# Kernel tuning notes

Measured on AMD Instinct MI355X. Metric: run time of the kernel, lower is better.

Reference implementation:

```python
import jax, jax.numpy as jnp
import numpy as np
from jax import lax

B_, H_, W_, C_ = 32, 56, 56, 256
RED = 16          # channel-attention reduction ratio
STATE = 16        # S6 state size
EPS = 1e-5        # BatchNorm eps


def setup_inputs() -> dict:
    key = jax.random.key(0)
    ks = jax.random.split(key, 10)
    x = jax.random.normal(ks[0], (B_, H_, W_, C_), jnp.float32)
    # ChannelAttention 1x1 convs (bias=False): C -> C/RED -> C
    ca_w1 = jax.random.normal(ks[1], (C_ // RED, C_), jnp.float32) * 0.05
    ca_w2 = jax.random.normal(ks[2], (C_, C_ // RED), jnp.float32) * 0.05
    # LSA 7x7 conv, 2 in-channels -> 1 out, HWIO layout
    lsa_w = jax.random.normal(ks[3], (7, 7, 2, 1), jnp.float32) * 0.05
    # S6 (d_model=1, state=STATE) parameters
    A = -jnp.exp(jax.random.normal(ks[4], (1, STATE), jnp.float32) * 0.5)  # negative for stable scan
    d_w = jax.random.normal(ks[5], (1, 1), jnp.float32) * 0.5
    d_b = jnp.zeros((1,), jnp.float32)
    B_w = jax.random.normal(ks[6], (STATE, 1), jnp.float32) * 0.5
    B_b = jnp.zeros((STATE,), jnp.float32)
    C_w = jax.random.normal(ks[7], (STATE, 1), jnp.float32) * 0.5
    C_b = jnp.zeros((STATE,), jnp.float32)
    bn_gamma = jnp.ones((C_,), jnp.float32)
    bn_beta = jnp.zeros((C_,), jnp.float32)
    return dict(x=x, ca_w1=ca_w1, ca_w2=ca_w2, lsa_w=lsa_w, A=A, d_w=d_w, d_b=d_b,
                B_w=B_w, B_b=B_b, C_w=C_w, C_b=C_b, bn_gamma=bn_gamma, bn_beta=bn_beta)


def _s6(m, A, d_w, d_b, B_w, B_b, C_w, C_b):
    # m: (B, L, 1) -- selective scan with d_model=1, state STATE
    delta = jax.nn.softplus(m @ d_w.T + d_b)          # (B,L,1)
    Bm = m @ B_w.T + B_b                              # (B,L,S)
    Cm = m @ C_w.T + C_b                              # (B,L,S)
    dA = jnp.exp(delta[..., None] * A)                # (B,L,1,S)
    dBx = (delta * m)[..., None] * Bm[:, :, None, :]  # (B,L,1,S)
    a_t = jnp.moveaxis(dA, 1, 0)                      # (L,B,1,S)
    b_t = jnp.moveaxis(dBx, 1, 0)
    c_t = jnp.moveaxis(Cm[:, :, None, :], 1, 0)       # (L,B,1,S)

    def step(h, abc):
        a, b, c = abc
        h = a * h + b                                 # (B,1,S)
        y = jnp.sum(h * c, axis=-1)                   # (B,1)
        return h, y

    h0 = jnp.zeros_like(a_t[0])
    _, ys = lax.scan(step, h0, (a_t, b_t, c_t))       # (L,B,1)
    return jnp.moveaxis(ys, 0, 1)                     # (B,L,1)


def reference(x, ca_w1, ca_w2, lsa_w, A, d_w, d_b, B_w, B_b, C_w, C_b, bn_gamma, bn_beta):
    Bn, H, W, C = x.shape
    # --- ChannelAttention (NHWC: reduce over spatial) ---
    avg = jnp.mean(x, axis=(1, 2))                    # (B,C)
    mx = jnp.max(x, axis=(1, 2))                      # (B,C)
    fc = lambda v: jax.nn.relu(v @ ca_w1.T) @ ca_w2.T
    ca_gate = jax.nn.sigmoid(fc(avg) + fc(mx))[:, None, None, :]
    xc = x * ca_gate                                  # (B,H,W,C)
    # --- GSA: channel-mean -> S6 over flattened spatial seq -> sigmoid gate ---
    m = jnp.mean(xc, axis=-1, keepdims=True).reshape(Bn, H * W, 1)
    y = _s6(m, A, d_w, d_b, B_w, B_b, C_w, C_b).reshape(Bn, H, W, 1)
    ma = xc * jax.nn.sigmoid(y)
    # --- LSA: [mean, max] over channels -> 7x7 conv -> sigmoid gate ---
    feat = jnp.concatenate([jnp.mean(xc, axis=-1, keepdims=True),
                            jnp.max(xc, axis=-1, keepdims=True)], axis=-1)  # (B,H,W,2)
    s = lax.conv_general_dilated(feat, lsa_w, (1, 1), 'SAME',
                                 dimension_numbers=('NHWC', 'HWIO', 'NHWC'))
    sa = xc * jax.nn.sigmoid(s)
    # --- sum, BatchNorm (training-mode batch stats over B,H,W), ReLU ---
    x2 = ma + sa
    mean = jnp.mean(x2, axis=(0, 1, 2))
    var = jnp.var(x2, axis=(0, 1, 2))
    out = (x2 - mean) * lax.rsqrt(var + EPS) * bn_gamma + bn_beta
    return jax.nn.relu(out)
```

## Files before the change

### kernel.cpp

```cpp
#include <hip/hip_runtime.h>
#include <math.h>

#define BB   32
#define HH   56
#define WWI  56
#define CC   256
#define LL   3136
#define SS   16
#define NCH  56
#define CHL  56
#define NSL  98
#define EPSV 1e-5f

__global__ void k_ca_partial(const float* __restrict__ x,
                             float* __restrict__ psum, float* __restrict__ pmax) {
    const int b = blockIdx.x, sl = blockIdx.y;
    const int wv = threadIdx.x >> 6, l = threadIdx.x & 63;
    const float4* x4 = (const float4*)x;
    const size_t base = ((size_t)b * LL + sl * 32) * 64;
    float4 s  = make_float4(0.f, 0.f, 0.f, 0.f);
    float4 mx = make_float4(-1e30f, -1e30f, -1e30f, -1e30f);
#pragma unroll
    for (int k = 0; k < 8; k++) {
        float4 v = x4[base + (size_t)(k * 4 + wv) * 64 + l];
        s.x += v.x; s.y += v.y; s.z += v.z; s.w += v.w;
        mx.x = fmaxf(mx.x, v.x); mx.y = fmaxf(mx.y, v.y);
        mx.z = fmaxf(mx.z, v.z); mx.w = fmaxf(mx.w, v.w);
    }
    __shared__ float4 ls[4][64], lm[4][64];
    ls[wv][l] = s; lm[wv][l] = mx;
    __syncthreads();
    if (wv == 0) {
#pragma unroll
        for (int w = 1; w < 4; w++) {
            float4 a = ls[w][l], m2 = lm[w][l];
            s.x += a.x; s.y += a.y; s.z += a.z; s.w += a.w;
            mx.x = fmaxf(mx.x, m2.x); mx.y = fmaxf(mx.y, m2.y);
            mx.z = fmaxf(mx.z, m2.z); mx.w = fmaxf(mx.w, m2.w);
        }
        ((float4*)psum)[(b * NSL + sl) * 64 + l] = s;
        ((float4*)pmax)[(b * NSL + sl) * 64 + l] = mx;
    }
}

__global__ void k_ca_fc(const float* __restrict__ psum, const float* __restrict__ pmax,
                        const float* __restrict__ w1, const float* __restrict__ w2,
                        float* __restrict__ gate) {
    const int b = blockIdx.x, tid = threadIdx.x;
    __shared__ float avg[CC], mxs[CC], hsum[16];
    float s = 0.f, mx = -1e30f;
    for (int k = 0; k < NSL; k++) {
        s += psum[(b * NSL + k) * CC + tid];
        mx = fmaxf(mx, pmax[(b * NSL + k) * CC + tid]);
    }
    avg[tid] = s * (1.f / 3136.f);
    mxs[tid] = mx;
    __syncthreads();
    const int r = tid >> 4, l = tid & 15;
    float pa = 0.f, pm = 0.f;
    for (int j = 0; j < 16; j++) {
        float w = w1[r * CC + l * 16 + j];
        pa += avg[l * 16 + j] * w;
        pm += mxs[l * 16 + j] * w;
    }
#pragma unroll
    for (int d = 1; d < 16; d <<= 1) { pa += __shfl_xor(pa, d); pm += __shfl_xor(pm, d); }
    if (l == 0) hsum[r] = fmaxf(pa, 0.f) + fmaxf(pm, 0.f);
    __syncthreads();
    float o = 0.f;
#pragma unroll
    for (int r2 = 0; r2 < 16; r2++) o += hsum[r2] * w2[tid * 16 + r2];
    gate[b * CC + tid] = 1.f / (1.f + __expf(-o));
}

__device__ __forceinline__ float softplusf(float z) {
    return fmaxf(z, 0.f) + __logf(1.f + __expf(-fabsf(z)));
}
__device__ __forceinline__ float sigmoidf(float z) {
    return 1.f / (1.f + __expf(-z));
}

__global__ void k_pos_reduce(const float* __restrict__ x, const float* __restrict__ gate,
                             const float* __restrict__ dw, const float* __restrict__ db,
                             float* __restrict__ m, float* __restrict__ cmax,
                             float4* __restrict__ mdd) {
    const int wv = threadIdx.x >> 6, l = threadIdx.x & 63;
    const int b = blockIdx.y;
    float4 g = ((const float4*)gate)[b * 64 + l];
    const float dwv = dw[0], dbv = db[0];
#pragma unroll
    for (int k = 0; k < 4; k++) {
        const int pos = b * LL + blockIdx.x * 16 + k * 4 + wv;
        float4 v = ((const float4*)x)[(size_t)pos * 64 + l];
        v.x *= g.x; v.y *= g.y; v.z *= g.z; v.w *= g.w;
        float s  = v.x + v.y + v.z + v.w;
        float mm = fmaxf(fmaxf(v.x, v.y), fmaxf(v.z, v.w));
#pragma unroll
        for (int d = 1; d < 64; d <<= 1) {
            s += __shfl_xor(s, d);
            mm = fmaxf(mm, __shfl_xor(mm, d));
        }
        if (l == 0) {
            float mv = s * (1.f / 256.f);
            m[pos] = mv;
            cmax[pos] = mm;
            float dl = softplusf(mv * dwv + dbv);
            mdd[pos] = make_float4(mv, dl, dl * mv, 0.f);
        }
    }
}

__global__ void k_gsa2(const float4* __restrict__ mdd,
                       const float* __restrict__ m, const float* __restrict__ cmax,
                       const float* __restrict__ Bw, const float* __restrict__ Bb,
                       const float* __restrict__ Cw, const float* __restrict__ Cb,
                       const float* __restrict__ A,  const float* __restrict__ wc,
                       float* __restrict__ sy, float* __restrict__ ssg) {
    __shared__ __align__(16) char smem[60928];
    const int tid = threadIdx.x;

    if (blockIdx.x < BB) {
        const int b = blockIdx.x;
        float4* mddl = (float4*)smem;
        float*  Pl   = (float*)(smem + 50176);
        float*  Ql   = (float*)(smem + 50176 + 3584);
        float*  hl   = (float*)(smem + 50176 + 7168);
        for (int i = tid; i < LL; i += 896) mddl[i] = mdd[b * LL + i];
        __syncthreads();

        const int g = tid >> 4, s = tid & 15;
        const float As = A[s], Bws = Bw[s], Bbs = Bb[s];
        const float Cws = Cw[s], Cbs = Cb[s];

        float sumd = 0.f, Q = 0.f;
        for (int t = 0; t < CHL; t++) {
            float4 md = mddl[g * CHL + t];
            float a = __expf(md.y * As);
            Q = a * Q + md.z * (md.x * Bws + Bbs);
            sumd += md.y;
        }
        Pl[g * 16 + s] = __expf(sumd * As);
        Ql[g * 16 + s] = Q;
        __syncthreads();

        if (g == 0) {
            float h = 0.f;
            for (int ch = 0; ch < NCH; ch++) {
                hl[ch * 16 + s] = h;
                h = Pl[ch * 16 + s] * h + Ql[ch * 16 + s];
            }
        }
        __syncthreads();

        float h = hl[g * 16 + s];
        for (int t = 0; t < CHL; t++) {
            float4 md = mddl[g * CHL + t];
            float a = __expf(md.y * As);
            h = a * h + md.z * (md.x * Bws + Bbs);
            float p = h * (md.x * Cws + Cbs);
#pragma unroll
            for (int d = 1; d < 16; d <<= 1) p += __shfl_xor(p, d);
            if (s == 0) sy[b * LL + g * CHL + t] = sigmoidf(p);
        }
    } else {
        const int b = blockIdx.x - BB;
        float* ml = (float*)smem;
        float* cl = (float*)(smem + 12544);
        float* wl = (float*)(smem + 25088);
        for (int i = tid; i < LL; i += 896) {
            ml[i] = m[b * LL + i];
            cl[i] = cmax[b * LL + i];
        }
        if (tid < 98) wl[tid] = wc[tid];
        __syncthreads();
        for (int pos = tid; pos < LL; pos += 896) {
            const int h0 = pos / WWI, w0 = pos - h0 * WWI;
            float acc = 0.f;
#pragma unroll
            for (int kh = 0; kh < 7; kh++) {
                int hh = h0 + kh - 3;
                if ((unsigned)hh >= (unsigned)HH) continue;
                const int rb = hh * WWI;
#pragma unroll
                for (int kw = 0; kw < 7; kw++) {
                    int ww = w0 + kw - 3;
                    if ((unsigned)ww >= (unsigned)WWI) continue;
                    acc += ml[rb + ww] * wl[(kh * 7 + kw) * 2]
                         + cl[rb + ww] * wl[(kh * 7 + kw) * 2 + 1];
                }
            }
            ssg[b * LL + pos] = sigmoidf(acc);
        }
    }
}

__global__ void k_bnstat(const float* __restrict__ x, const float* __restrict__ gate,
                         const float* __restrict__ sy, const float* __restrict__ ssg,
                         float* __restrict__ pb) {
    const int b = blockIdx.x, sl = blockIdx.y;
    const int wv = threadIdx.x >> 6, l = threadIdx.x & 63;
    const float4* x4 = (const float4*)x;
    float4 g = ((const float4*)gate)[b * 64 + l];
    float4 s = make_float4(0.f, 0.f, 0.f, 0.f);
    float4 q = make_float4(0.f, 0.f, 0.f, 0.f);
#pragma unroll
    for (int k = 0; k < 8; k++) {
        int pos = b * LL + sl * 32 + k * 4 + wv;
        float4 v = x4[(size_t)pos * 64 + l];
        float g2 = sy[pos] + ssg[pos];
        float fx = v.x * g.x * g2, fy = v.y * g.y * g2, fz = v.z * g.z * g2, fw = v.w * g.w * g2;
        s.x += fx; s.y += fy; s.z += fz; s.w += fw;
        q.x += fx * fx; q.y += fy * fy; q.z += fz * fz; q.w += fw * fw;
    }
    __shared__ float4 ls[4][64], lq[4][64];
    ls[wv][l] = s; lq[wv][l] = q;
    __syncthreads();
    if (wv == 0) {
#pragma unroll
        for (int w = 1; w < 4; w++) {
            float4 a = ls[w][l], c = lq[w][l];
            s.x += a.x; s.y += a.y; s.z += a.z; s.w += a.w;
            q.x += c.x; q.y += c.y; q.z += c.z; q.w += c.w;
        }
        ((float4*)pb)[(b * NSL + sl) * 128 + l] = s;
        ((float4*)pb)[(b * NSL + sl) * 128 + 64 + l] = q;
    }
}

__global__ void k_bnfin(const float* __restrict__ pb,
                        const float* __restrict__ gamma, const float* __restrict__ beta,
                        float* __restrict__ sc, float* __restrict__ sh) {
    const int c = blockIdx.x;
    const int tid = threadIdx.x;
    float s0 = 0.f, q0 = 0.f;
    for (int sl = tid; sl < BB * NSL; sl += 256) {
        s0 += pb[(size_t)sl * 512 + c];
        q0 += pb[(size_t)sl * 512 + 256 + c];
    }
    __shared__ float rs[256], rq[256];
    rs[tid] = s0; rq[tid] = q0;
    __syncthreads();
    for (int d = 128; d > 0; d >>= 1) {
        if (tid < d) { rs[tid] += rs[tid + d]; rq[tid] += rq[tid + d]; }
        __syncthreads();
    }
    if (tid == 0) {
        const float inv = 1.f / (float)(BB * LL);
        float mean = rs[0] * inv;
        float var  = rq[0] * inv - mean * mean;
        float sv = gamma[c] * rsqrtf(var + EPSV);
        sc[c] = sv;
        sh[c] = beta[c] - mean * sv;
    }
}

__global__ void k_final(const float* __restrict__ x, const float* __restrict__ gate,
                        const float* __restrict__ sy, const float* __restrict__ ssg,
                        const float* __restrict__ sc, const float* __restrict__ sh,
                        float* __restrict__ out) {
    const int wv = threadIdx.x >> 6, l = threadIdx.x & 63;
    const int b = blockIdx.y;
    const float4 scv = ((const float4*)sc)[l];
    const float4 shv = ((const float4*)sh)[l];
    const float4 g = ((const float4*)gate)[b * 64 + l];
#pragma unroll
    for (int k = 0; k < 4; k++) {
        const int pos = b * LL + blockIdx.x * 16 + k * 4 + wv;
        float4 v = ((const float4*)x)[(size_t)pos * 64 + l];
        float g2 = sy[pos] + ssg[pos];
        float4 o;
        o.x = fmaxf(v.x * g.x * g2 * scv.x + shv.x, 0.f);
        o.y = fmaxf(v.y * g.y * g2 * scv.y + shv.y, 0.f);
        o.z = fmaxf(v.z * g.z * g2 * scv.z + shv.z, 0.f);
        o.w = fmaxf(v.w * g.w * g2 * scv.w + shv.w, 0.f);
        ((float4*)out)[(size_t)pos * 64 + l] = o;
    }
}

extern "C" void kernel_launch(void* const* d_in, const int* in_sizes, int n_in,
                              void* d_out, int out_size, void* d_ws, size_t ws_size,
                              hipStream_t stream) {
    const float* x     = (const float*)d_in[0];
    const float* ca_w1 = (const float*)d_in[1];
    const float* ca_w2 = (const float*)d_in[2];
    const float* lsa_w = (const float*)d_in[3];
    const float* A     = (const float*)d_in[4];
    const float* d_wp  = (const float*)d_in[5];
    const float* d_bp  = (const float*)d_in[6];
    const float* B_wp  = (const float*)d_in[7];
    const float* B_bp  = (const float*)d_in[8];
    const float* C_wp  = (const float*)d_in[9];
    const float* C_bp  = (const float*)d_in[10];
    const float* bn_g  = (const float*)d_in[11];
    const float* bn_b  = (const float*)d_in[12];
    float* out = (float*)d_out;

    float* psum = out;
    float* pmax = psum + BB * NSL * CC;
    float* pb   = pmax + BB * NSL * CC;

    float* ws    = (float*)d_ws;
    float* gate  = ws;
    float* m     = gate  + 8192;
    float* cmax  = m     + 100352;
    float* sy    = cmax  + 100352;
    float* ssg   = sy    + 100352;
    float4* mdd  = (float4*)(ssg + 100352);
    float* scv   = (float*)(mdd + 100352);
    float* shv   = scv   + 256;

    k_ca_partial<<<dim3(BB, NSL), 256, 0, stream>>>(x, psum, pmax);
    k_ca_fc<<<BB, 256, 0, stream>>>(psum, pmax, ca_w1, ca_w2, gate);
    k_pos_reduce<<<dim3(LL / 16, BB), 256, 0, stream>>>(x, gate, d_wp, d_bp, m, cmax, mdd);
    k_gsa2<<<2 * BB, 896, 0, stream>>>(mdd, m, cmax, B_wp, B_bp, C_wp, C_bp, A, lsa_w, sy, ssg);
    k_bnstat<<<dim3(BB, NSL), 256, 0, stream>>>(x, gate, sy, ssg, pb);
    k_bnfin<<<CC, 256, 0, stream>>>(pb, bn_g, bn_b, scv, shv);
    k_final<<<dim3(LL / 16, BB), 256, 0, stream>>>(x, gate, sy, ssg, scv, shv, out);
}
```

Measured before the change: 131.3 us.

## Fuse all stages into one cooperative persistent kernel with grid syncs

Replaces the seven separate kernel launches with a single cooperative persistent kernel that walks through every stage and separates them with grid-wide barriers. Channel reduction, the gate MLP, the position reduction, the chunked S6 scan (split into chunk-summary, carry-propagation and re-scan phases spread across waves), the 7x7 conv, the BN statistics and the final output all run inside it. The aim is to remove launch gaps and tail effects between the small stages. The cost is eight grid syncs, a serial carry phase on only 8 waves, and the scan and conv now reading from global memory instead of LDS. The old multi-kernel path remains as a fallback if the cooperative launch fails.

```diff
diff --git a/kernel.cpp b/kernel.cpp
--- a/kernel.cpp
+++ b/kernel.cpp
@@ -1,16 +1,276 @@
 #include <hip/hip_runtime.h>
+#include <hip/hip_cooperative_groups.h>
 #include <math.h>
 
+namespace cg = cooperative_groups;
+
 #define BB   32
-#define HH   56
+#define HHI  56
 #define WWI  56
 #define CC   256
 #define LL   3136
 #define SS   16
 #define NCH  56
 #define CHL  56
+#define WPP  16
+#define NU   (BB * LL / WPP)
 #define NSL  98
 #define EPSV 1e-5f
+
+__device__ __forceinline__ float softplusf(float z) {
+    return fmaxf(z, 0.f) + __logf(1.f + __expf(-fabsf(z)));
+}
+__device__ __forceinline__ float sigmoidf(float z) {
+    return 1.f / (1.f + __expf(-z));
+}
+
+struct KParams {
+    const float *x, *ca_w1, *ca_w2, *lsa_w, *A, *dw, *db, *Bw, *Bb, *Cw, *Cb, *bng, *bnb;
+    float *out;
+    float4 *mdd;
+    float *gate, *m, *cmax, *sy, *ssg, *scv, *shv, *Pp, *Qq, *hst, *psum, *pmax, *pb;
+};
+
+__global__ __launch_bounds__(512, 4) void k_mega(KParams p) {
+    cg::grid_group gridg = cg::this_grid();
+    const int tid  = threadIdx.x;
+    const int lane = tid & 63;
+    const int wv   = tid >> 6;
+    const int gw   = blockIdx.x * 8 + wv;
+    const int NW   = gridDim.x * 8;
+    const float4* x4 = (const float4*)p.x;
+
+    __shared__ float s_avg[2][CC], s_mxs[2][CC], s_h[2][16];
+    __shared__ float s_bn[16][2];
+
+    for (int u = gw; u < NU; u += NW) {
+        int b  = u / (LL / WPP);
+        int sl = u - b * (LL / WPP);
+        size_t base = ((size_t)b * LL + sl * WPP) * 64 + lane;
+        float4 s  = make_float4(0.f, 0.f, 0.f, 0.f);
+        float4 mx = make_float4(-1e30f, -1e30f, -1e30f, -1e30f);
+#pragma unroll
+        for (int k = 0; k < WPP; k++) {
+            float4 v = x4[base + (size_t)k * 64];
+            s.x += v.x; s.y += v.y; s.z += v.z; s.w += v.w;
+            mx.x = fmaxf(mx.x, v.x); mx.y = fmaxf(mx.y, v.y);
+            mx.z = fmaxf(mx.z, v.z); mx.w = fmaxf(mx.w, v.w);
+        }
+        ((float4*)p.psum)[(size_t)u * 64 + lane] = s;
+        ((float4*)p.pmax)[(size_t)u * 64 + lane] = mx;
+    }
+    gridg.sync();
+
+    if (blockIdx.x < 16) {
+        const int half = tid >> 8;
+        const int c    = tid & 255;
+        const int b    = blockIdx.x * 2 + half;
+        float s = 0.f, mx = -1e30f;
+        for (int k = 0; k < 196; k++) {
+            s  += p.psum[(b * 196 + k) * 256 + c];
+            mx = fmaxf(mx, p.pmax[(b * 196 + k) * 256 + c]);
+        }
+        s_avg[half][c] = s * (1.f / 3136.f);
+        s_mxs[half][c] = mx;
+        __syncthreads();
+        const int r = c >> 4, l = c & 15;
+        float pa = 0.f, pm = 0.f;
+        for (int j = 0; j < 16; j++) {
+            float w = p.ca_w1[r * 256 + l * 16 + j];
+            pa += s_avg[half][l * 16 + j] * w;
+            pm += s_mxs[half][l * 16 + j] * w;
+        }
+#pragma unroll
+        for (int d = 1; d < 16; d <<= 1) { pa += __shfl_xor(pa, d); pm += __shfl_xor(pm, d); }
+        if (l == 0) s_h[half][r] = fmaxf(pa, 0.f) + fmaxf(pm, 0.f);
+        __syncthreads();
+        float o = 0.f;
+#pragma unroll
+        for (int r2 = 0; r2 < 16; r2++) o += s_h[half][r2] * p.ca_w2[c * 16 + r2];
+        p.gate[b * 256 + c] = sigmoidf(o);
+    }
+    gridg.sync();
+
+    {
+        const float dwv = p.dw[0], dbv = p.db[0];
+        for (int u = gw; u < BB * LL / 4; u += NW) {
+            int p0 = u * 4;
+            int b = p0 / LL;
+            float4 g = ((const float4*)p.gate)[b * 64 + lane];
+#pragma unroll
+            for (int k = 0; k < 4; k++) {
+                int pos = p0 + k;
+                float4 v = x4[(size_t)pos * 64 + lane];
+                v.x *= g.x; v.y *= g.y; v.z *= g.z; v.w *= g.w;
+                float s  = v.x + v.y + v.z + v.w;
+                float mm = fmaxf(fmaxf(v.x, v.y), fmaxf(v.z, v.w));
+#pragma unroll
+                for (int d = 1; d < 64; d <<= 1) {
+                    s += __shfl_xor(s, d);
+                    mm = fmaxf(mm, __shfl_xor(mm, d));
+                }
+                if (lane == 0) {
+                    float mv = s * (1.f / 256.f);
+                    p.m[pos] = mv;
+                    p.cmax[pos] = mm;
+                    float dl = softplusf(mv * dwv + dbv);
+                    p.mdd[pos] = make_float4(mv, dl, dl * mv, 0.f);
+                }
+            }
+        }
+    }
+    gridg.sync();
+
+    {
+        const int sub = lane >> 4, s = lane & 15;
+        const float As = p.A[s], Bws = p.Bw[s], Bbs = p.Bb[s];
+        for (int q = gw; q < 448; q += NW) {
+            int gidx = q * 4 + sub;
+            int b = gidx / NCH, ch = gidx - b * NCH;
+            int base = b * LL + ch * CHL;
+            float sumd = 0.f, Q = 0.f;
+            for (int t = 0; t < CHL; t++) {
+                float4 md = p.mdd[base + t];
+                float a = __expf(md.y * As);
+                Q = a * Q + md.z * (md.x * Bws + Bbs);
+                sumd += md.y;
+            }
+            int idx = ch * 512 + b * 16 + s;
+            p.Pp[idx] = __expf(sumd * As);
+            p.Qq[idx] = Q;
+        }
+    }
+    gridg.sync();
+
+    if (gw < 8) {
+        const int bsub = lane >> 4, s = lane & 15;
+        const int b = gw * 4 + bsub;
+        float h = 0.f;
+        for (int ch = 0; ch < NCH; ch++) {
+            int idx = ch * 512 + b * 16 + s;
+            p.hst[idx] = h;
+            h = p.Pp[idx] * h + p.Qq[idx];
+        }
+    }
+    gridg.sync();
+
+    {
+        const int sub = lane >> 4, s = lane & 15;
+        if (gw < 448) {
+            const float As = p.A[s], Bws = p.Bw[s], Bbs = p.Bb[s];
+            const float Cws = p.Cw[s], Cbs = p.Cb[s];
+            for (int q = gw; q < 448; q += NW) {
+                int gidx = q * 4 + sub;
+                int b = gidx / NCH, ch = gidx - b * NCH;
+                int base = b * LL + ch * CHL;
+                float h = p.hst[ch * 512 + b * 16 + s];
+                for (int t = 0; t < CHL; t++) {
+                    float4 md = p.mdd[base + t];
+                    float a = __expf(md.y * As);
+                    h = a * h + md.z * (md.x * Bws + Bbs);
+                    float pr = h * (md.x * Cws + Cbs);
+#pragma unroll
+                    for (int d = 1; d < 16; d <<= 1) pr += __shfl_xor(pr, d);
+                    if (s == 0) p.sy[base + t] = sigmoidf(pr);
+                }
+            }
+        } else {
+            for (int w2 = gw - 448; w2 < 1568; w2 += NW - 448) {
+                int pos = w2 * 64 + lane;
+                int b = pos / LL;
+                int ii = pos - b * LL;
+                int h0 = ii / WWI, w0 = ii - h0 * WWI;
+                const float* mb = p.m + b * LL;
+                const float* cb = p.cmax + b * LL;
+                float acc = 0.f;
+#pragma unroll
+                for (int kh = 0; kh < 7; kh++) {
+                    int hh = h0 + kh - 3;
+                    if ((unsigned)hh >= (unsigned)HHI) continue;
+                    int rb = hh * WWI;
+#pragma unroll
+                    for (int kw = 0; kw < 7; kw++) {
+                        int ww = w0 + kw - 3;
+                        if ((unsigned)ww >= (unsigned)WWI) continue;
+                        acc += mb[rb + ww] * p.lsa_w[(kh * 7 + kw) * 2]
+                             + cb[rb + ww] * p.lsa_w[(kh * 7 + kw) * 2 + 1];
+                    }
+                }
+                p.ssg[pos] = sigmoidf(acc);
+            }
+        }
+    }
+    gridg.sync();
+
+    for (int u = gw; u < NU; u += NW) {
+        int b  = u / (LL / WPP);
+        int sl = u - b * (LL / WPP);
+        int pos0 = b * LL + sl * WPP;
+        float4 g = ((const float4*)p.gate)[b * 64 + lane];
+        float4 s = make_float4(0.f, 0.f, 0.f, 0.f);
+        float4 q = make_float4(0.f, 0.f, 0.f, 0.f);
+#pragma unroll
+        for (int k = 0; k < WPP; k++) {
+            int pos = pos0 + k;
+            float4 v = x4[(size_t)pos * 64 + lane];
+            float g2 = p.sy[pos] + p.ssg[pos];
+            float fx = v.x * g.x * g2, fy = v.y * g.y * g2;
+            float fz = v.z * g.z * g2, fw = v.w * g.w * g2;
+            s.x += fx; s.y += fy; s.z += fz; s.w += fw;
+            q.x += fx * fx; q.y += fy * fy; q.z += fz * fz; q.w += fw * fw;
+        }
+        ((float4*)p.pb)[(size_t)u * 128 + lane]      = s;
+        ((float4*)p.pb)[(size_t)u * 128 + 64 + lane] = q;
+    }
+    gridg.sync();
+
+    if (blockIdx.x < 16) {
+        const int rep   = tid & 15;
+        const int kind  = (tid >> 4) & 1;
+        const int c_loc = tid >> 5;
+        const int col   = kind * 256 + blockIdx.x * 16 + c_loc;
+        float acc = 0.f;
+        for (int k = 0; k < 392; k++) {
+            acc += p.pb[(size_t)(rep + k * 16) * 512 + col];
+        }
+#pragma unroll
+        for (int d = 1; d < 16; d <<= 1) acc += __shfl_xor(acc, d);
+        if (rep == 0) s_bn[c_loc][kind] = acc;
+        __syncthreads();
+        if (tid < 16) {
+            const int c = blockIdx.x * 16 + tid;
+            const float inv = 1.f / (float)(BB * LL);
+            float mean = s_bn[tid][0] * inv;
+            float var  = s_bn[tid][1] * inv - mean * mean;
+            float sv = p.bng[c] * rsqrtf(var + EPSV);
+            p.scv[c] = sv;
+            p.shv[c] = p.bnb[c] - mean * sv;
+        }
+    }
+    gridg.sync();
+
+    {
+        float4 scv4 = ((const float4*)p.scv)[lane];
+        float4 shv4 = ((const float4*)p.shv)[lane];
+        for (int u = gw; u < BB * LL / 4; u += NW) {
+            int p0 = u * 4;
+            int b = p0 / LL;
+            float4 g = ((const float4*)p.gate)[b * 64 + lane];
+#pragma unroll
+            for (int k = 0; k < 4; k++) {
+                int pos = p0 + k;
+                float4 v = x4[(size_t)pos * 64 + lane];
+                float g2 = p.sy[pos] + p.ssg[pos];
+                float4 o;
+                o.x = fmaxf(v.x * g.x * g2 * scv4.x + shv4.x, 0.f);
+                o.y = fmaxf(v.y * g.y * g2 * scv4.y + shv4.y, 0.f);
+                o.z = fmaxf(v.z * g.z * g2 * scv4.z + shv4.z, 0.f);
+                o.w = fmaxf(v.w * g.w * g2 * scv4.w + shv4.w, 0.f);
+                ((float4*)p.out)[(size_t)pos * 64 + lane] = o;
+            }
+        }
+    }
+}
 
 __global__ void k_ca_partial(const float* __restrict__ x,
                              float* __restrict__ psum, float* __restrict__ pmax) {
@@ -70,14 +330,7 @@
     float o = 0.f;
 #pragma unroll
     for (int r2 = 0; r2 < 16; r2++) o += hsum[r2] * w2[tid * 16 + r2];
-    gate[b * CC + tid] = 1.f / (1.f + __expf(-o));
-}
-
-__device__ __forceinline__ float softplusf(float z) {
-    return fmaxf(z, 0.f) + __logf(1.f + __expf(-fabsf(z)));
-}
-__device__ __forceinline__ float sigmoidf(float z) {
-    return 1.f / (1.f + __expf(-z));
+    gate[b * CC + tid] = sigmoidf(o);
 }
 
 __global__ void k_pos_reduce(const float* __restrict__ x, const float* __restrict__ gate,
@@ -118,7 +371,6 @@
                        float* __restrict__ sy, float* __restrict__ ssg) {
     __shared__ __align__(16) char smem[60928];
     const int tid = threadIdx.x;
-
     if (blockIdx.x < BB) {
         const int b = blockIdx.x;
         float4* mddl = (float4*)smem;
@@ -127,11 +379,9 @@
         float*  hl   = (float*)(smem + 50176 + 7168);
         for (int i = tid; i < LL; i += 896) mddl[i] = mdd[b * LL + i];
         __syncthreads();
-
         const int g = tid >> 4, s = tid & 15;
         const float As = A[s], Bws = Bw[s], Bbs = Bb[s];
         const float Cws = Cw[s], Cbs = Cb[s];
-
         float sumd = 0.f, Q = 0.f;
         for (int t = 0; t < CHL; t++) {
             float4 md = mddl[g * CHL + t];
@@ -142,7 +392,6 @@
         Pl[g * 16 + s] = __expf(sumd * As);
         Ql[g * 16 + s] = Q;
         __syncthreads();
-
         if (g == 0) {
             float h = 0.f;
             for (int ch = 0; ch < NCH; ch++) {
@@ -151,7 +400,6 @@
             }
         }
         __syncthreads();
-
         float h = hl[g * 16 + s];
         for (int t = 0; t < CHL; t++) {
             float4 md = mddl[g * CHL + t];
@@ -179,7 +427,7 @@
 #pragma unroll
             for (int kh = 0; kh < 7; kh++) {
                 int hh = h0 + kh - 3;
-                if ((unsigned)hh >= (unsigned)HH) continue;
+                if ((unsigned)hh >= (unsigned)HHI) continue;
                 const int rb = hh * WWI;
 #pragma unroll
                 for (int kw = 0; kw < 7; kw++) {
@@ -295,25 +543,47 @@
     const float* bn_b  = (const float*)d_in[12];
     float* out = (float*)d_out;
 
-    float* psum = out;
-    float* pmax = psum + BB * NSL * CC;
-    float* pb   = pmax + BB * NSL * CC;
-
-    float* ws    = (float*)d_ws;
-    float* gate  = ws;
-    float* m     = gate  + 8192;
-    float* cmax  = m     + 100352;
-    float* sy    = cmax  + 100352;
-    float* ssg   = sy    + 100352;
-    float4* mdd  = (float4*)(ssg + 100352);
-    float* scv   = (float*)(mdd + 100352);
-    float* shv   = scv   + 256;
-
-    k_ca_partial<<<dim3(BB, NSL), 256, 0, stream>>>(x, psum, pmax);
-    k_ca_fc<<<BB, 256, 0, stream>>>(psum, pmax, ca_w1, ca_w2, gate);
-    k_pos_reduce<<<dim3(LL / 16, BB), 256, 0, stream>>>(x, gate, d_wp, d_bp, m, cmax, mdd);
-    k_gsa2<<<2 * BB, 896, 0, stream>>>(mdd, m, cmax, B_wp, B_bp, C_wp, C_bp, A, lsa_w, sy, ssg);
-    k_bnstat<<<dim3(BB, NSL), 256, 0, stream>>>(x, gate, sy, ssg, pb);
-    k_bnfin<<<CC, 256, 0, stream>>>(pb, bn_g, bn_b, scv, shv);
-    k_final<<<dim3(LL / 16, BB), 256, 0, stream>>>(x, gate, sy, ssg, scv, shv, out);
-}
+    float* ws = (float*)d_ws;
+    float4* mdd  = (float4*)ws;
+    float* gate  = ws + 401408;
+    float* m     = gate + 8192;
+    float* cmax  = m + 100352;
+    float* sy    = cmax + 100352;
+    float* ssg   = sy + 100352;
+    float* scv   = ssg + 100352;
+    float* shv   = scv + 256;
+    float* Pp    = shv + 256;
+    float* Qq    = Pp + 28672;
+    float* hst   = Qq + 28672;
+    float* psum  = hst + 28672;
+    float* pmax  = psum + 1605632;
+    float* pb    = pmax + 1605632;
+
+    KParams kp;
+    kp.x = x; kp.ca_w1 = ca_w1; kp.ca_w2 = ca_w2; kp.lsa_w = lsa_w; kp.A = A;
+    kp.dw = d_wp; kp.db = d_bp; kp.Bw = B_wp; kp.Bb = B_bp; kp.Cw = C_wp; kp.Cb = C_bp;
+    kp.bng = bn_g; kp.bnb = bn_b; kp.out = out;
+    kp.mdd = mdd; kp.gate = gate; kp.m = m; kp.cmax = cmax; kp.sy = sy; kp.ssg = ssg;
+    kp.scv = scv; kp.shv = shv; kp.Pp = Pp; kp.Qq = Qq; kp.hst = hst;
+    kp.psum = psum; kp.pmax = pmax; kp.pb = pb;
+
+    int maxb = 0;
+    hipError_t e = hipOccupancyMaxActiveBlocksPerMultiprocessor(&maxb, k_mega, 512, 0);
+    if (e != hipSuccess || maxb < 1) maxb = 1;
+    int grid = maxb * 256;
+    if (grid > 1024) grid = 1024;
+
+    void* args[] = { (void*)&kp };
+    e = hipLaunchCooperativeKernel((const void*)k_mega, dim3(grid), dim3(512),
+                                   args, 0, stream);
+    if (e != hipSuccess) {
+        (void)hipGetLastError();
+        k_ca_partial<<<dim3(BB, NSL), 256, 0, stream>>>(x, psum, pmax);
+        k_ca_fc<<<BB, 256, 0, stream>>>(psum, pmax, ca_w1, ca_w2, gate);
+        k_pos_reduce<<<dim3(LL / 16, BB), 256, 0, stream>>>(x, gate, d_wp, d_bp, m, cmax, mdd);
+        k_gsa2<<<2 * BB, 896, 0, stream>>>(mdd, m, cmax, B_wp, B_bp, C_wp, C_bp, A, lsa_w, sy, ssg);
+        k_bnstat<<<dim3(BB, NSL), 256, 0, stream>>>(x, gate, sy, ssg, pb);
+        k_bnfin<<<CC, 256, 0, stream>>>(pb, bn_g, bn_b, scv, shv);
+        k_final<<<dim3(LL / 16, BB), 256, 0, stream>>>(x, gate, sy, ssg, scv, shv, out);
+    }
+}
```

New measurement: 506.8 us. 3.86x slower.
